# Kernel tuning notes

Hardware: AMD Instinct MI355X
Metric: run time of the kernel (lower is better)

Reference implementation:

```python
import jax, jax.numpy as jnp
import numpy as np

TEMP = 0.05
EPS = 1e-8  # torch CosineSimilarity eps

def _l2_normalize(x):
    # matches torch: x / max(||x||, eps)
    n = jnp.sqrt(jnp.sum(x * x, axis=-1, keepdims=True))
    return x / jnp.maximum(n, EPS)

def setup_inputs() -> dict:
    key = jax.random.key(0)
    k1, k2, k3 = jax.random.split(key, 3)
    N, D = 8192, 256
    return {
        "anc": jax.random.normal(k1, (N, D), dtype=jnp.float32),
        "pos": jax.random.normal(k2, (N, D), dtype=jnp.float32),
        "neg": jax.random.normal(k3, (N, D), dtype=jnp.float32),
    }

def reference(anc, pos, neg):
    a = _l2_normalize(anc)            # [N, D]
    p = _l2_normalize(pos)            # [N, D]
    n = _l2_normalize(neg)            # [N, D]
    pos_sim = jnp.einsum('id,jd->ij', a, p) / TEMP   # [N, N]
    neg_sim = jnp.einsum('id,jd->ij', a, n) / TEMP   # [N, N]
    logits = jnp.concatenate([pos_sim, neg_sim], axis=1)  # [N, 2N]
    N_ = logits.shape[0]
    logp = jax.nn.log_softmax(logits, axis=-1)
    labels = jnp.arange(N_)
    # CrossEntropyLoss with mean reduction
    return -jnp.mean(logp[labels, labels])
```

## Files before the change

### kernel.cpp

```cpp
#include <hip/hip_runtime.h>
#include <hip/hip_bf16.h>

#define N_ROWS 8192
#define DIM 256
#define TEMP_INV 20.0f
#define C2F 1.7889516e-3f

typedef __attribute__((ext_vector_type(4))) int i32x4;

__global__ void __launch_bounds__(256) prep_kernel(
    const float* __restrict__ anc, const float* __restrict__ pos,
    const float* __restrict__ neg, char* __restrict__ a8,
    char* __restrict__ p8, char* __restrict__ n8,
    float* __restrict__ diag, float* __restrict__ rowsum,
    float* __restrict__ out) {
  __shared__ __align__(16) char t8[8192];
  const int lane = threadIdx.x & 63;
  const int w = threadIdx.x >> 6;

  if (blockIdx.x < 2048) {
    int wid = blockIdx.x * 4 + w;
    float4 a = reinterpret_cast<const float4*>(anc + (size_t)wid * DIM)[lane];
    float4 p = reinterpret_cast<const float4*>(pos + (size_t)wid * DIM)[lane];
    float d  = a.x * p.x + a.y * p.y + a.z * p.z + a.w * p.w;
    float na = a.x * a.x + a.y * a.y + a.z * a.z + a.w * a.w;
    float np = p.x * p.x + p.y * p.y + p.z * p.z + p.w * p.w;
#pragma unroll
    for (int m = 32; m; m >>= 1) {
      d  += __shfl_xor(d, m);
      na += __shfl_xor(na, m);
      np += __shfl_xor(np, m);
    }
    float rna = fmaxf(sqrtf(na), 1e-8f);
    float s = 127.0f / rna;
    int q0 = (int)rintf(a.x * s), q1 = (int)rintf(a.y * s);
    int q2 = (int)rintf(a.z * s), q3 = (int)rintf(a.w * s);
    unsigned pk = (q0 & 0xFF) | ((q1 & 0xFF) << 8) |
                  ((q2 & 0xFF) << 16) | ((q3 & 0xFF) << 24);
    *reinterpret_cast<unsigned*>(a8 + (size_t)wid * DIM + (lane << 2)) = pk;
    if (lane == 0) {
      diag[wid] = TEMP_INV * d / (rna * fmaxf(sqrtf(np), 1e-8f));
      rowsum[wid] = 0.f;
    }
    return;
  }
  const int b = blockIdx.x - 2048;
  if (b == 511 && threadIdx.x == 0) out[0] = 0.f;
  const float* src = (b < 256) ? pos : neg;
  char* dst = (b < 256) ? p8 : n8;
  const int pb = b & 255;
#pragma unroll
  for (int i = 0; i < 8; ++i) {
    int r = i * 4 + w;
    float4 v = reinterpret_cast<const float4*>(src + (size_t)(pb * 32 + r) * DIM)[lane];
    float ss = v.x * v.x + v.y * v.y + v.z * v.z + v.w * v.w;
#pragma unroll
    for (int m = 32; m; m >>= 1) ss += __shfl_xor(ss, m);
    float s = 127.0f / fmaxf(sqrtf(ss), 1e-8f);
    int q0 = (int)rintf(v.x * s), q1 = (int)rintf(v.y * s);
    int q2 = (int)rintf(v.z * s), q3 = (int)rintf(v.w * s);
    unsigned pk = (q0 & 0xFF) | ((q1 & 0xFF) << 8) |
                  ((q2 & 0xFF) << 16) | ((q3 & 0xFF) << 24);
    *reinterpret_cast<unsigned*>(t8 + ((lane >> 2) << 9) + (r << 4) +
                                 ((lane & 3) << 2)) = pk;
  }
  __syncthreads();
  const uint4* ts = reinterpret_cast<const uint4*>(t8);
  uint4* outp = reinterpret_cast<uint4*>(dst + (size_t)pb * 8192);
  outp[threadIdx.x]       = ts[threadIdx.x];
  outp[threadIdx.x + 256] = ts[threadIdx.x + 256];
}

__global__ void __launch_bounds__(256, 6) fused_kernel(
    const char* __restrict__ a8, const char* __restrict__ p8,
    const char* __restrict__ n8, float* __restrict__ rowsum) {
  __shared__ __align__(16) char smem[3 * 8192];
  const int tid  = threadIdx.x;
  const int lane = tid & 63;
  const int w    = tid >> 6;
  const int rb   = blockIdx.x >> 5;
  const int cc   = blockIdx.x & 31;
  const char* B = (cc < 16) ? (p8 + (size_t)cc * 16 * 8192)
                            : (n8 + (size_t)(cc - 16) * 16 * 8192);
  const int row0 = rb * 128 + w * 32;
  const int ar = lane & 15;
  const int g  = lane >> 4;
  const int vbase = (g << 9) + (ar << 4);

  i32x4 af[2][4];
#pragma unroll
  for (int rf = 0; rf < 2; ++rf)
#pragma unroll
    for (int km = 0; km < 4; ++km) {
      af[rf][km] = *reinterpret_cast<const i32x4*>(
          a8 + (size_t)(row0 + rf * 16 + ar) * DIM + km * 64 + g * 16);
      asm volatile("" : "+v"(af[rf][km]));
    }

#define STAGE(slot, p)                                                         \
  {                                                                            \
    _Pragma("unroll")                                                          \
    for (int j = 0; j < 2; ++j) {                                              \
      const int L = (w << 1) | j;                                              \
      const char* src = B + ((size_t)(p) << 13) + (L << 10) + (lane << 4);     \
      char* dst = (char*)smem + ((slot) << 13) + (L << 10);                    \
      __builtin_amdgcn_global_load_lds(                                        \
          (const __attribute__((address_space(1))) void*)src,                  \
          (__attribute__((address_space(3))) void*)dst, 16, 0, 0);             \
    }                                                                          \
  }

#define MMI(A, Bf, C) __builtin_amdgcn_mfma_i32_16x16x64_i8((A), (Bf), (C), 0, 0, 0)

#define CLUSTER(CFOFF)                                                         \
  {                                                                            \
    i32x4 bf[4];                                                               \
    _Pragma("unroll")                                                          \
    for (int km = 0; km < 4; ++km)                                             \
      bf[km] = *reinterpret_cast<const i32x4*>(pbase + (km << 11) + (CFOFF));  \
    i32x4 acc[2];                                                              \
    _Pragma("unroll")                                                          \
    for (int rf = 0; rf < 2; ++rf) acc[rf] = MMI(af[rf][0], bf[0], zeroi);     \
    _Pragma("unroll")                                                          \
    for (int km = 1; km < 4; ++km)                                             \
      _Pragma("unroll")                                                        \
      for (int rf = 0; rf < 2; ++rf)                                           \
        acc[rf] = MMI(af[rf][km], bf[km], acc[rf]);                            \
    _Pragma("unroll")                                                          \
    for (int rf = 0; rf < 2; ++rf)                                             \
      _Pragma("unroll")                                                        \
      for (int q = 0; q < 4; ++q)                                              \
        psum[rf][q] += __builtin_amdgcn_exp2f((float)acc[rf][q] * C2F);        \
  }

  float psum[2][4];
#pragma unroll
  for (int rf = 0; rf < 2; ++rf)
#pragma unroll
    for (int q = 0; q < 4; ++q) psum[rf][q] = 0.f;
  const i32x4 zeroi = {0, 0, 0, 0};

  STAGE(0, 0);
  STAGE(1, 1);
  int rd = 0;
  for (int it = 0; it < 16; ++it) {
    if (it <= 14) asm volatile("s_waitcnt vmcnt(2)" ::: "memory");
    else          asm volatile("s_waitcnt vmcnt(0)" ::: "memory");
    __builtin_amdgcn_s_barrier();
    const char* pbase = smem + (rd << 13) + vbase;
    const int st = (rd == 0) ? 2 : rd - 1;
    CLUSTER(0);
    if (it <= 13) STAGE(st, it + 2);
    CLUSTER(256);
    rd = (rd == 2) ? 0 : rd + 1;
  }

#pragma unroll
  for (int rf = 0; rf < 2; ++rf)
#pragma unroll
    for (int q = 0; q < 4; ++q) {
      float s = psum[rf][q];
      s += __shfl_xor(s, 1);
      s += __shfl_xor(s, 2);
      s += __shfl_xor(s, 4);
      s += __shfl_xor(s, 8);
      if (ar == 0)
        atomicAdd(rowsum + row0 + rf * 16 + g * 4 + q, s);
    }
#undef STAGE
#undef CLUSTER
#undef MMI
}

__global__ void __launch_bounds__(512) loss_kernel(
    const float* __restrict__ rowsum, const float* __restrict__ diag,
    float* __restrict__ out) {
  __shared__ float sh[8];
  int i = blockIdx.x * 512 + threadIdx.x;
  float acc = logf(rowsum[i]) - diag[i];
#pragma unroll
  for (int m = 32; m; m >>= 1) acc += __shfl_xor(acc, m);
  if ((threadIdx.x & 63) == 0) sh[threadIdx.x >> 6] = acc;
  __syncthreads();
  if (threadIdx.x == 0) {
    float t = 0.f;
#pragma unroll
    for (int j = 0; j < 8; ++j) t += sh[j];
    atomicAdd(out, t / (float)N_ROWS);
  }
}

extern "C" void kernel_launch(void* const* d_in, const int* in_sizes, int n_in,
                              void* d_out, int out_size, void* d_ws, size_t ws_size,
                              hipStream_t stream) {
  const float* anc = (const float*)d_in[0];
  const float* pos = (const float*)d_in[1];
  const float* neg = (const float*)d_in[2];
  char* ws = (char*)d_ws;
  char* a8 = ws;
  char* p8 = ws + (size_t)N_ROWS * DIM;
  char* n8 = p8 + (size_t)N_ROWS * DIM;
  float* diag = (float*)(ws + (size_t)3 * N_ROWS * DIM);
  float* rowsum = diag + N_ROWS;
  float* out = (float*)d_out;

  prep_kernel<<<2048 + 512, 256, 0, stream>>>(anc, pos, neg, a8, p8, n8, diag, rowsum, out);
  fused_kernel<<<64 * 32, 256, 0, stream>>>(a8, p8, n8, rowsum);
  loss_kernel<<<16, 512, 0, stream>>>(rowsum, diag, out);
}
```

Baseline: 57.20 us.

## Switch fused GEMM-logsumexp to 32x32x32 int8 MFMA with single accumulator

Replaces the pairs of 16x16x64 int8 MFMAs (two row fragments, two column clusters per stage) with one 32x32x32 int8 MFMA chain per stage. Each wave now covers a 32x32 output tile with 8 chained K-steps and one 16-element accumulator. The A-fragment and LDS B-fragment layouts and the final row reduction and atomic indexing are rewritten to match, and the occupancy hint drops from 6 to 5. The aim is fewer MFMA issues and fewer LDS reads per tile, at the cost of a longer dependent MFMA chain and higher register pressure.

```diff
diff --git a/kernel.cpp b/kernel.cpp
--- a/kernel.cpp
+++ b/kernel.cpp
@@ -7,6 +7,7 @@
 #define C2F 1.7889516e-3f
 
 typedef __attribute__((ext_vector_type(4))) int i32x4;
+typedef __attribute__((ext_vector_type(16))) int i32x16;
 
 __global__ void __launch_bounds__(256) prep_kernel(
     const float* __restrict__ anc, const float* __restrict__ pos,
@@ -71,7 +72,7 @@
   outp[threadIdx.x + 256] = ts[threadIdx.x + 256];
 }
 
-__global__ void __launch_bounds__(256, 6) fused_kernel(
+__global__ void __launch_bounds__(256, 5) fused_kernel(
     const char* __restrict__ a8, const char* __restrict__ p8,
     const char* __restrict__ n8, float* __restrict__ rowsum) {
   __shared__ __align__(16) char smem[3 * 8192];
@@ -83,19 +84,17 @@
   const char* B = (cc < 16) ? (p8 + (size_t)cc * 16 * 8192)
                             : (n8 + (size_t)(cc - 16) * 16 * 8192);
   const int row0 = rb * 128 + w * 32;
-  const int ar = lane & 15;
-  const int g  = lane >> 4;
-  const int vbase = (g << 9) + (ar << 4);
-
-  i32x4 af[2][4];
-#pragma unroll
-  for (int rf = 0; rf < 2; ++rf)
-#pragma unroll
-    for (int km = 0; km < 4; ++km) {
-      af[rf][km] = *reinterpret_cast<const i32x4*>(
-          a8 + (size_t)(row0 + rf * 16 + ar) * DIM + km * 64 + g * 16);
-      asm volatile("" : "+v"(af[rf][km]));
-    }
+  const int cr = lane & 31;
+  const int hi = lane >> 5;
+  const int vbase = (hi << 9) + (cr << 4);
+
+  i32x4 af[8];
+#pragma unroll
+  for (int km = 0; km < 8; ++km) {
+    af[km] = *reinterpret_cast<const i32x4*>(
+        a8 + (size_t)(row0 + cr) * DIM + km * 32 + hi * 16);
+    asm volatile("" : "+v"(af[km]));
+  }
 
 #define STAGE(slot, p)                                                         \
   {                                                                            \
@@ -110,35 +109,12 @@
     }                                                                          \
   }
 
-#define MMI(A, Bf, C) __builtin_amdgcn_mfma_i32_16x16x64_i8((A), (Bf), (C), 0, 0, 0)
-
-#define CLUSTER(CFOFF)                                                         \
-  {                                                                            \
-    i32x4 bf[4];                                                               \
-    _Pragma("unroll")                                                          \
-    for (int km = 0; km < 4; ++km)                                             \
-      bf[km] = *reinterpret_cast<const i32x4*>(pbase + (km << 11) + (CFOFF));  \
-    i32x4 acc[2];                                                              \
-    _Pragma("unroll")                                                          \
-    for (int rf = 0; rf < 2; ++rf) acc[rf] = MMI(af[rf][0], bf[0], zeroi);     \
-    _Pragma("unroll")                                                          \
-    for (int km = 1; km < 4; ++km)                                             \
-      _Pragma("unroll")                                                        \
-      for (int rf = 0; rf < 2; ++rf)                                           \
-        acc[rf] = MMI(af[rf][km], bf[km], acc[rf]);                            \
-    _Pragma("unroll")                                                          \
-    for (int rf = 0; rf < 2; ++rf)                                             \
-      _Pragma("unroll")                                                        \
-      for (int q = 0; q < 4; ++q)                                              \
-        psum[rf][q] += __builtin_amdgcn_exp2f((float)acc[rf][q] * C2F);        \
-  }
-
-  float psum[2][4];
-#pragma unroll
-  for (int rf = 0; rf < 2; ++rf)
-#pragma unroll
-    for (int q = 0; q < 4; ++q) psum[rf][q] = 0.f;
-  const i32x4 zeroi = {0, 0, 0, 0};
+#define MMI(A, Bf, C) __builtin_amdgcn_mfma_i32_32x32x32_i8((A), (Bf), (C), 0, 0, 0)
+
+  float psum[16];
+#pragma unroll
+  for (int e = 0; e < 16; ++e) psum[e] = 0.f;
+  const i32x16 zeroi = {0, 0, 0, 0, 0, 0, 0, 0, 0, 0, 0, 0, 0, 0, 0, 0};
 
   STAGE(0, 0);
   STAGE(1, 1);
@@ -149,26 +125,46 @@
     __builtin_amdgcn_s_barrier();
     const char* pbase = smem + (rd << 13) + vbase;
     const int st = (rd == 0) ? 2 : rd - 1;
-    CLUSTER(0);
+    i32x16 acc;
+    {
+      i32x4 b0 = *reinterpret_cast<const i32x4*>(pbase);
+      i32x4 b1 = *reinterpret_cast<const i32x4*>(pbase + 1024);
+      i32x4 b2 = *reinterpret_cast<const i32x4*>(pbase + 2048);
+      i32x4 b3 = *reinterpret_cast<const i32x4*>(pbase + 3072);
+      acc = MMI(af[0], b0, zeroi);
+      acc = MMI(af[1], b1, acc);
+      acc = MMI(af[2], b2, acc);
+      acc = MMI(af[3], b3, acc);
+    }
     if (it <= 13) STAGE(st, it + 2);
-    CLUSTER(256);
+    {
+      i32x4 b4 = *reinterpret_cast<const i32x4*>(pbase + 4096);
+      i32x4 b5 = *reinterpret_cast<const i32x4*>(pbase + 5120);
+      i32x4 b6 = *reinterpret_cast<const i32x4*>(pbase + 6144);
+      i32x4 b7 = *reinterpret_cast<const i32x4*>(pbase + 7168);
+      acc = MMI(af[4], b4, acc);
+      acc = MMI(af[5], b5, acc);
+      acc = MMI(af[6], b6, acc);
+      acc = MMI(af[7], b7, acc);
+    }
+#pragma unroll
+    for (int e = 0; e < 16; ++e)
+      psum[e] += __builtin_amdgcn_exp2f((float)acc[e] * C2F);
     rd = (rd == 2) ? 0 : rd + 1;
   }
 
 #pragma unroll
-  for (int rf = 0; rf < 2; ++rf)
-#pragma unroll
-    for (int q = 0; q < 4; ++q) {
-      float s = psum[rf][q];
-      s += __shfl_xor(s, 1);
-      s += __shfl_xor(s, 2);
-      s += __shfl_xor(s, 4);
-      s += __shfl_xor(s, 8);
-      if (ar == 0)
-        atomicAdd(rowsum + row0 + rf * 16 + g * 4 + q, s);
-    }
+  for (int e = 0; e < 16; ++e) {
+    float s = psum[e];
+    s += __shfl_xor(s, 1);
+    s += __shfl_xor(s, 2);
+    s += __shfl_xor(s, 4);
+    s += __shfl_xor(s, 8);
+    s += __shfl_xor(s, 16);
+    if (cr == 0)
+      atomicAdd(rowsum + row0 + (e & 3) + 8 * (e >> 2) + 4 * hi, s);
+  }
 #undef STAGE
-#undef CLUSTER
 #undef MMI
 }
 
```

After: 70.88 us. +23.9%, slower.
